# Kernel tuning notes

Measured on AMD Instinct MI355X. Metric: run time of the kernel, lower is better.

Reference implementation:

```python
import jax, jax.numpy as jnp
import numpy as np

N_HEAD = 12
N_EMBD = 768


def setup_inputs() -> dict:
    key = jax.random.key(0)
    k1, k2, k3, k4, k5 = jax.random.split(key, 5)
    B, T, C = 4, 2048, N_EMBD
    s = 0.02
    x = jax.random.normal(k1, (B, T, C), dtype=jnp.float32)
    w_attn = jax.random.normal(k2, (C, 3 * C), dtype=jnp.float32) * s
    b_attn = jnp.zeros((3 * C,), dtype=jnp.float32)
    w_proj = jax.random.normal(k3, (C, C), dtype=jnp.float32) * s
    b_proj = jnp.zeros((C,), dtype=jnp.float32)
    return {"x": x, "w_attn": w_attn, "b_attn": b_attn, "w_proj": w_proj, "b_proj": b_proj}


def reference(x, w_attn, b_attn, w_proj, b_proj):
    # dropout omitted (eval mode / dropout=0.0)
    B, T, C = x.shape
    H = N_HEAD
    D = C // H  # head dim
    qkv = x @ w_attn + b_attn                      # [B,T,3C]
    q, k, v = jnp.split(qkv, 3, axis=-1)
    q = q.reshape(B, T, H, D).transpose(0, 2, 1, 3)  # [B,H,T,D]
    k = k.reshape(B, T, H, D).transpose(0, 2, 1, 3)
    v = v.reshape(B, T, H, D).transpose(0, 2, 1, 3)
    att = jnp.einsum('bhqd,bhkd->bhqk', q, k) * (1.0 / np.sqrt(D))  # [B,H,T,T]
    causal = jnp.tril(jnp.ones((T, T), dtype=bool))
    att = jnp.where(causal[None, None], att, -jnp.inf)
    att = jax.nn.softmax(att, axis=-1)
    y = jnp.einsum('bhqk,bhkd->bhqd', att, v)      # [B,H,T,D]
    y = y.transpose(0, 2, 1, 3).reshape(B, T, C)
    return y @ w_proj + b_proj
```

## Files before the change

kernel.cpp:

```cpp
#include <hip/hip_runtime.h>
#include <stdint.h>

typedef unsigned short ushort_t;

#define T_SEQ 2048
#define BATCH 4
#define NHEAD 12
#define CEMB 768
#define HDIM 64
#define C3 2304

__device__ __forceinline__ ushort_t f2b_hw(float f) {
  union { __bf16 h; ushort_t u; } p;
  p.h = (__bf16)f;
  return p.u;
}
__device__ __forceinline__ uint32_t pkbf16(float lo, float hi) {
  union { __bf16 h[2]; uint32_t u; } p;
  p.h[0] = (__bf16)lo; p.h[1] = (__bf16)hi;
  return p.u;
}

typedef __attribute__((address_space(3))) unsigned int lds_u32_t;
typedef const __attribute__((address_space(1))) unsigned int glb_u32_t;
__device__ __forceinline__ void async_cp16(const void* g, void* l) {
  __builtin_amdgcn_global_load_lds((glb_u32_t*)g, (lds_u32_t*)l, 16, 0, 0);
}

__global__ __launch_bounds__(256) void prep_k(const float* __restrict__ x, ushort_t* __restrict__ xb,
                                              const float* __restrict__ wa, ushort_t* __restrict__ wT,
                                              const float* __restrict__ wp, ushort_t* __restrict__ wpT) {
  const int blk = blockIdx.x;
  const int tid = threadIdx.x;
  if (blk < 3072) {
    const int i = blk * 256 + tid;
    float4 a = ((const float4*)x)[2 * i];
    float4 b = ((const float4*)x)[2 * i + 1];
    uint4 v;
    v.x = pkbf16(a.x, a.y); v.y = pkbf16(a.z, a.w);
    v.z = pkbf16(b.x, b.y); v.w = pkbf16(b.z, b.w);
    ((uint4*)xb)[i] = v;
    return;
  }
  __shared__ ushort_t tile[32][33];
  const float* in; ushort_t* out; int R, C, bx, by;
  if (blk < 4800) {
    const int t = blk - 3072;
    in = wa; out = wT; R = CEMB; C = C3;
    bx = t % 72; by = t / 72;
  } else {
    const int t = blk - 4800;
    in = wp; out = wpT; R = CEMB; C = CEMB;
    bx = t % 24; by = t / 24;
  }
  const int tx = tid & 31, ty = tid >> 5;
  const int c0 = bx * 32, r0 = by * 32;
  for (int i = ty; i < 32; i += 8)
    tile[i][tx] = f2b_hw(in[(size_t)(r0 + i) * C + c0 + tx]);
  __syncthreads();
  for (int i = ty; i < 32; i += 8)
    out[(size_t)(c0 + i) * R + r0 + tx] = tile[tx][i];
}

typedef __bf16 bf16x8 __attribute__((ext_vector_type(8)));
typedef float f32x4 __attribute__((ext_vector_type(4)));

template <bool OUTF, int BM>
__global__ __launch_bounds__(256) void gemm_bt(const ushort_t* __restrict__ A,
                                               const ushort_t* __restrict__ Bt,
                                               const float* __restrict__ bias,
                                               void* __restrict__ Cv,
                                               int M, int N, int K) {
  constexpr int TM = BM / 32;
  __shared__ ushort_t As[2 * BM * 32];
  __shared__ ushort_t Bs[2 * 128 * 32];
  const int tid = threadIdx.x;
  const int m0 = blockIdx.y * BM, n0 = blockIdx.x * 128;
  const int wid = tid >> 6, lane = tid & 63;
  const int quad = lane >> 4, l15 = lane & 15;
  const int wm = (wid >> 1) * (BM / 2), wn = (wid & 1) * 64;
  f32x4 acc[TM][4] = {};

  const int e0 = tid * 8;
  const int r0s = e0 >> 5, c0s = e0 & 31;
  const int e1 = e0 + 2048;
  const int r1s = e1 >> 5, c1s = e1 & 31;

  for (int k0 = 0; k0 < K; k0 += 64) {
    __syncthreads();
#pragma unroll
    for (int p = 0; p < 2; p++) {
      const int kc = k0 + p * 32;
      async_cp16(&A[(size_t)(m0 + r0s) * K + kc + c0s], &As[p * BM * 32 + e0]);
      if constexpr (BM == 128)
        async_cp16(&A[(size_t)(m0 + r1s) * K + kc + c1s], &As[p * BM * 32 + e1]);
      async_cp16(&Bt[(size_t)(n0 + r0s) * K + kc + c0s], &Bs[p * 128 * 32 + e0]);
      async_cp16(&Bt[(size_t)(n0 + r1s) * K + kc + c1s], &Bs[p * 128 * 32 + e1]);
    }
    __syncthreads();
    bf16x8 af[TM][2], bfr[4][2];
#pragma unroll
    for (int t = 0; t < TM; t++)
#pragma unroll
      for (int p = 0; p < 2; p++)
        af[t][p] = *(const bf16x8*)&As[p * BM * 32 + (wm + t * 16 + l15) * 32 + quad * 8];
#pragma unroll
    for (int t = 0; t < 4; t++)
#pragma unroll
      for (int p = 0; p < 2; p++)
        bfr[t][p] = *(const bf16x8*)&Bs[p * 128 * 32 + (wn + t * 16 + l15) * 32 + quad * 8];
#pragma unroll
    for (int p = 0; p < 2; p++)
#pragma unroll
      for (int tm = 0; tm < TM; tm++)
#pragma unroll
        for (int tn = 0; tn < 4; tn++)
          acc[tm][tn] = __builtin_amdgcn_mfma_f32_16x16x32_bf16(af[tm][p], bfr[tn][p], acc[tm][tn], 0, 0, 0);
  }

#pragma unroll
  for (int tm = 0; tm < TM; tm++) {
    const int row = m0 + wm + tm * 16 + quad * 4;
#pragma unroll
    for (int tn = 0; tn < 4; tn++) {
      const int col = n0 + wn + tn * 16 + l15;
      const float bv = bias[col];
#pragma unroll
      for (int rr = 0; rr < 4; rr++) {
        if constexpr (OUTF)
          ((float*)Cv)[(size_t)(row + rr) * N + col] = acc[tm][tn][rr] + bv;
        else
          ((ushort_t*)Cv)[(size_t)(row + rr) * N + col] = f2b_hw(acc[tm][tn][rr] + bv);
      }
    }
  }
}

#define VSTR 64

__device__ __forceinline__ void commit_v(ushort_t* __restrict__ vt, const int* __restrict__ offs,
                                         uint4 pV0, uint4 pV1) {
  union { uint32_t u[4]; uint4 v; } a, c;
  a.v = pV0; c.v = pV1;
#pragma unroll
  for (int j = 0; j < 8; j++) {
    uint32_t pk = __builtin_amdgcn_perm(c.u[j >> 1], a.u[j >> 1],
                                        (j & 1) ? 0x07060302u : 0x05040100u);
    *(uint32_t*)&vt[offs[j]] = pk;
  }
}

__global__ __launch_bounds__(256) void attn_mfma_k(const ushort_t* __restrict__ qkv,
                                                   ushort_t* __restrict__ y) {
  __shared__ ushort_t Ksm[2][2][64 * 32];
  __shared__ ushort_t Vt[2][64 * VSTR];
  __shared__ ushort_t Plds[4][16 * VSTR];

  const int qt = 31 - blockIdx.y;
  const int h = blockIdx.x >> 2, b = blockIdx.x & 3;
  const int tid = threadIdx.x;
  const int w = tid >> 6, lane = tid & 63;
  const int quad = lane >> 4, l15 = lane & 15;
  const int nkt = qt + 1;
  const int qw = qt * 64 + w * 16;

  const int e0 = tid * 8;
  const int kchunk = (tid & 3) ^ ((tid >> 3) & 3);
  const ushort_t* kbase = qkv + ((size_t)(b * T_SEQ) + (tid >> 2)) * C3 + CEMB + h * HDIM + kchunk * 8;
  const int vpair = tid & 31, vd0 = (tid >> 5) * 8;
  const ushort_t* vbase = qkv + ((size_t)(b * T_SEQ) + 2 * vpair) * C3 + 2 * CEMB + h * HDIM + vd0;
  const size_t step = (size_t)64 * C3;

  int voffw[8];
#pragma unroll
  for (int j = 0; j < 8; j++)
    voffw[j] = (vd0 + j) * VSTR + (((vpair >> 2) ^ j) << 3) + ((vpair & 3) << 1);

  const int sw7 = l15 & 7;
  int koff[4];
#pragma unroll
  for (int m = 0; m < 4; m++)
    koff[m] = (m * 16 + l15) * 32 + ((quad ^ ((l15 >> 1) & 3)) << 3);
  int apoff[2];
#pragma unroll
  for (int kb = 0; kb < 2; kb++)
    apoff[kb] = l15 * VSTR + (((quad + 4 * kb) ^ sw7) << 3);
  int poffWm[4];
#pragma unroll
  for (int m = 0; m < 4; m++)
    poffWm[m] = l15 * VSTR + (((2 * m + (quad >> 1)) ^ sw7) << 3) + ((quad & 1) << 2);
  const int qloc = 16 * w + l15;

  const float C2 = 0.18033688011112042f;

  bf16x8 qB[2];
#pragma unroll
  for (int kb = 0; kb < 2; kb++)
    qB[kb] = *(const bf16x8*)&qkv[((size_t)(b * T_SEQ + qw + l15)) * C3 +
                                  h * HDIM + kb * 32 + quad * 8];

  f32x4 o2[4] = {};
  float m_i = -3e38f, l_i = 0.f;

  const ushort_t* kp = kbase;
  const ushort_t* vp = vbase;
  uint4 pV0 = *(const uint4*)vp, pV1 = *(const uint4*)(vp + C3);
  async_cp16(kp, &Ksm[0][0][e0]);
  async_cp16(kp + 32, &Ksm[0][1][e0]);
  commit_v(Vt[0], voffw, pV0, pV1);
  vp += step;
  pV0 = *(const uint4*)vp; pV1 = *(const uint4*)(vp + C3);

  for (int kt = 0; kt < nkt; ++kt) {
    __syncthreads();
    if (kt + 1 < nkt) {
      const int nb = (kt + 1) & 1;
      kp += step;
      async_cp16(kp, &Ksm[nb][0][e0]);
      async_cp16(kp + 32, &Ksm[nb][1][e0]);
      commit_v(Vt[nb], voffw, pV0, pV1);
      if (kt + 2 < nkt) {
        vp += step;
        pV0 = *(const uint4*)vp; pV1 = *(const uint4*)(vp + C3);
      }
    }
    const int cb = kt & 1;

    bf16x8 kA[4][2];
#pragma unroll
    for (int m = 0; m < 4; m++) {
      kA[m][0] = *(const bf16x8*)&Ksm[cb][0][koff[m]];
      kA[m][1] = *(const bf16x8*)&Ksm[cb][1][koff[m]];
    }
    f32x4 st[4] = {};
#pragma unroll
    for (int m = 0; m < 4; m++) {
      st[m] = __builtin_amdgcn_mfma_f32_16x16x32_bf16(kA[m][0], qB[0], st[m], 0, 0, 0);
      st[m] = __builtin_amdgcn_mfma_f32_16x16x32_bf16(kA[m][1], qB[1], st[m], 0, 0, 0);
    }

    if (kt == qt) {
#pragma unroll
      for (int m = 0; m < 4; m++)
#pragma unroll
        for (int r = 0; r < 4; r++)
          if (m * 16 + quad * 4 + r > qloc) st[m][r] = -3e38f;
    }

    f32x4 mq;
#pragma unroll
    for (int r = 0; r < 4; r++)
      mq[r] = fmaxf(fmaxf(st[0][r], st[1][r]), fmaxf(st[2][r], st[3][r]));
    const float mxl = fmaxf(fmaxf(mq[0], mq[1]), fmaxf(mq[2], mq[3]));

    float al = 1.f;
    if (!__all(mxl - m_i <= 22.18f)) {
      float mx = fmaxf(mxl, __shfl_xor(mxl, 16, 64));
      mx = fmaxf(mx, __shfl_xor(mx, 32, 64));
      const float mnew = fmaxf(m_i, mx);
      al = exp2f((m_i - mnew) * C2);
      m_i = mnew;
#pragma unroll
      for (int nd = 0; nd < 4; nd++)
#pragma unroll
        for (int r = 0; r < 4; r++) o2[nd][r] *= al;
    }
    const float mnc = m_i * C2;
#pragma unroll
    for (int m = 0; m < 4; m++)
#pragma unroll
      for (int r = 0; r < 4; r++)
        st[m][r] = exp2f(fmaf(st[m][r], C2, -mnc));
    f32x4 s4;
#pragma unroll
    for (int r = 0; r < 4; r++)
      s4[r] = (st[0][r] + st[1][r]) + (st[2][r] + st[3][r]);
    float ls = (s4[0] + s4[1]) + (s4[2] + s4[3]);
    ls += __shfl_xor(ls, 16, 64);
    ls += __shfl_xor(ls, 32, 64);
    l_i = l_i * al + ls;

#pragma unroll
    for (int m = 0; m < 4; m++) {
      uint2 pk;
      pk.x = pkbf16(st[m][0], st[m][1]);
      pk.y = pkbf16(st[m][2], st[m][3]);
      *(uint2*)&Plds[w][poffWm[m]] = pk;
    }

    asm volatile("s_waitcnt lgkmcnt(0)" ::: "memory");

    bf16x8 ap[2], bv[4][2];
#pragma unroll
    for (int kb = 0; kb < 2; kb++)
      ap[kb] = *(const bf16x8*)&Plds[w][apoff[kb]];
#pragma unroll
    for (int nd = 0; nd < 4; nd++)
#pragma unroll
      for (int kb = 0; kb < 2; kb++)
        bv[nd][kb] = *(const bf16x8*)&Vt[cb][nd * 1024 + apoff[kb]];
#pragma unroll
    for (int nd = 0; nd < 4; nd++) {
      o2[nd] = __builtin_amdgcn_mfma_f32_16x16x32_bf16(bv[nd][0], ap[0], o2[nd], 0, 0, 0);
      o2[nd] = __builtin_amdgcn_mfma_f32_16x16x32_bf16(bv[nd][1], ap[1], o2[nd], 0, 0, 0);
    }
  }

  {
    const float inv = 1.0f / l_i;
    const int qg = qw + l15;
    ushort_t* yp = y + ((size_t)(b * T_SEQ + qg)) * CEMB + h * HDIM + quad * 4;
#pragma unroll
    for (int nd = 0; nd < 4; nd++) {
      uint2 pk;
      pk.x = pkbf16(o2[nd][0] * inv, o2[nd][1] * inv);
      pk.y = pkbf16(o2[nd][2] * inv, o2[nd][3] * inv);
      *(uint2*)(yp + nd * 16) = pk;
    }
  }
}

extern "C" void kernel_launch(void* const* d_in, const int* in_sizes, int n_in,
                              void* d_out, int out_size, void* d_ws, size_t ws_size,
                              hipStream_t stream) {
  const float* x      = (const float*)d_in[0];
  const float* w_attn = (const float*)d_in[1];
  const float* b_attn = (const float*)d_in[2];
  const float* w_proj = (const float*)d_in[3];
  const float* b_proj = (const float*)d_in[4];
  float* out = (float*)d_out;

  char* ws = (char*)d_ws;
  ushort_t* qkv = (ushort_t*)ws;
  ushort_t* y   = qkv + (size_t)8192 * 2304;
  ushort_t* xb  = y + (size_t)8192 * 768;
  ushort_t* wT  = xb + (size_t)8192 * 768;
  ushort_t* wpT = wT + (size_t)2304 * 768;

  prep_k<<<5376, 256, 0, stream>>>(x, xb, w_attn, wT, w_proj, wpT);

  gemm_bt<false, 128><<<dim3(C3 / 128, 8192 / 128), 256, 0, stream>>>(xb, wT, b_attn, qkv, 8192, C3, CEMB);

  attn_mfma_k<<<dim3(48, 32), 256, 0, stream>>>(qkv, y);

  gemm_bt<true, 64><<<dim3(CEMB / 128, 8192 / 64), 256, 0, stream>>>(y, wpT, b_proj, out, 8192, CEMB, CEMB);
}
```

Before: 231.1 us.

## Process 128 queries per attention block, two 16-row fragments per wave

The attention kernel now gives each wave 32 query rows, as two 16-row fragments, so each block covers 128 queries. Each K/V tile staged in LDS is reused for twice as many queries, which halves the grid and the K/V global traffic per query. The row-sum reduction across lanes is deferred to the epilogue, and a launch-bounds occupancy hint is added. In exchange there is higher register and LDS pressure, fewer blocks for load balancing across the causal triangle, and wasted masked work on the last two diagonal tiles.

```diff
diff --git a/kernel.cpp b/kernel.cpp
--- a/kernel.cpp
+++ b/kernel.cpp
@@ -150,19 +150,19 @@
   }
 }
 
-__global__ __launch_bounds__(256) void attn_mfma_k(const ushort_t* __restrict__ qkv,
-                                                   ushort_t* __restrict__ y) {
+__global__ __launch_bounds__(256, 3) void attn_mfma_k(const ushort_t* __restrict__ qkv,
+                                                      ushort_t* __restrict__ y) {
   __shared__ ushort_t Ksm[2][2][64 * 32];
   __shared__ ushort_t Vt[2][64 * VSTR];
-  __shared__ ushort_t Plds[4][16 * VSTR];
-
-  const int qt = 31 - blockIdx.y;
+  __shared__ ushort_t Plds[4][32 * VSTR];
+
+  const int qt = 15 - blockIdx.y;
   const int h = blockIdx.x >> 2, b = blockIdx.x & 3;
   const int tid = threadIdx.x;
   const int w = tid >> 6, lane = tid & 63;
   const int quad = lane >> 4, l15 = lane & 15;
-  const int nkt = qt + 1;
-  const int qw = qt * 64 + w * 16;
+  const int nkt = 2 * qt + 2;
+  const int qw = qt * 128 + w * 32;
 
   const int e0 = tid * 8;
   const int kchunk = (tid & 3) ^ ((tid >> 3) & 3);
@@ -181,26 +181,33 @@
 #pragma unroll
   for (int m = 0; m < 4; m++)
     koff[m] = (m * 16 + l15) * 32 + ((quad ^ ((l15 >> 1) & 3)) << 3);
-  int apoff[2];
+  int vroff[2];
 #pragma unroll
   for (int kb = 0; kb < 2; kb++)
-    apoff[kb] = l15 * VSTR + (((quad + 4 * kb) ^ sw7) << 3);
-  int poffWm[4];
-#pragma unroll
-  for (int m = 0; m < 4; m++)
-    poffWm[m] = l15 * VSTR + (((2 * m + (quad >> 1)) ^ sw7) << 3) + ((quad & 1) << 2);
-  const int qloc = 16 * w + l15;
+    vroff[kb] = l15 * VSTR + (((quad + 4 * kb) ^ sw7) << 3);
+  int poffW[2][4];
+#pragma unroll
+  for (int qf = 0; qf < 2; qf++)
+#pragma unroll
+    for (int m = 0; m < 4; m++)
+      poffW[qf][m] = (qf * 16 + l15) * VSTR + (((2 * m + (quad >> 1)) ^ sw7) << 3) + ((quad & 1) << 2);
+
+  const int qrel0 = w * 32 + l15;
+  const int qrel1 = qrel0 + 16;
 
   const float C2 = 0.18033688011112042f;
 
-  bf16x8 qB[2];
-#pragma unroll
-  for (int kb = 0; kb < 2; kb++)
-    qB[kb] = *(const bf16x8*)&qkv[((size_t)(b * T_SEQ + qw + l15)) * C3 +
-                                  h * HDIM + kb * 32 + quad * 8];
-
-  f32x4 o2[4] = {};
-  float m_i = -3e38f, l_i = 0.f;
+  bf16x8 qB[2][2];
+#pragma unroll
+  for (int qf = 0; qf < 2; qf++)
+#pragma unroll
+    for (int kb = 0; kb < 2; kb++)
+      qB[qf][kb] = *(const bf16x8*)&qkv[((size_t)(b * T_SEQ + qw + qf * 16 + l15)) * C3 +
+                                        h * HDIM + kb * 32 + quad * 8];
+
+  f32x4 o2[2][4] = {};
+  float m0 = -3e38f, m1 = -3e38f;
+  float lq0 = 0.f, lq1 = 0.f;
 
   const ushort_t* kp = kbase;
   const ushort_t* vp = vbase;
@@ -232,90 +239,123 @@
       kA[m][0] = *(const bf16x8*)&Ksm[cb][0][koff[m]];
       kA[m][1] = *(const bf16x8*)&Ksm[cb][1][koff[m]];
     }
-    f32x4 st[4] = {};
+    f32x4 st0[4] = {}, st1[4] = {};
 #pragma unroll
     for (int m = 0; m < 4; m++) {
-      st[m] = __builtin_amdgcn_mfma_f32_16x16x32_bf16(kA[m][0], qB[0], st[m], 0, 0, 0);
-      st[m] = __builtin_amdgcn_mfma_f32_16x16x32_bf16(kA[m][1], qB[1], st[m], 0, 0, 0);
-    }
-
-    if (kt == qt) {
+      st0[m] = __builtin_amdgcn_mfma_f32_16x16x32_bf16(kA[m][0], qB[0][0], st0[m], 0, 0, 0);
+      st0[m] = __builtin_amdgcn_mfma_f32_16x16x32_bf16(kA[m][1], qB[0][1], st0[m], 0, 0, 0);
+      st1[m] = __builtin_amdgcn_mfma_f32_16x16x32_bf16(kA[m][0], qB[1][0], st1[m], 0, 0, 0);
+      st1[m] = __builtin_amdgcn_mfma_f32_16x16x32_bf16(kA[m][1], qB[1][1], st1[m], 0, 0, 0);
+    }
+
+    if (kt >= nkt - 2) {
+      const int krel = (kt << 6) - (qt << 7) + quad * 4;
 #pragma unroll
       for (int m = 0; m < 4; m++)
 #pragma unroll
-        for (int r = 0; r < 4; r++)
-          if (m * 16 + quad * 4 + r > qloc) st[m][r] = -3e38f;
-    }
-
-    f32x4 mq;
-#pragma unroll
-    for (int r = 0; r < 4; r++)
-      mq[r] = fmaxf(fmaxf(st[0][r], st[1][r]), fmaxf(st[2][r], st[3][r]));
-    const float mxl = fmaxf(fmaxf(mq[0], mq[1]), fmaxf(mq[2], mq[3]));
-
-    float al = 1.f;
-    if (!__all(mxl - m_i <= 22.18f)) {
-      float mx = fmaxf(mxl, __shfl_xor(mxl, 16, 64));
-      mx = fmaxf(mx, __shfl_xor(mx, 32, 64));
-      const float mnew = fmaxf(m_i, mx);
-      al = exp2f((m_i - mnew) * C2);
-      m_i = mnew;
+        for (int r = 0; r < 4; r++) {
+          const int kr = krel + m * 16 + r;
+          if (kr > qrel0) st0[m][r] = -3e38f;
+          if (kr > qrel1) st1[m][r] = -3e38f;
+        }
+    }
+
+    f32x4 mq0, mq1;
+#pragma unroll
+    for (int r = 0; r < 4; r++) {
+      mq0[r] = fmaxf(fmaxf(st0[0][r], st0[1][r]), fmaxf(st0[2][r], st0[3][r]));
+      mq1[r] = fmaxf(fmaxf(st1[0][r], st1[1][r]), fmaxf(st1[2][r], st1[3][r]));
+    }
+    const float mx0 = fmaxf(fmaxf(mq0[0], mq0[1]), fmaxf(mq0[2], mq0[3]));
+    const float mx1 = fmaxf(fmaxf(mq1[0], mq1[1]), fmaxf(mq1[2], mq1[3]));
+
+    float al0 = 1.f, al1 = 1.f;
+    const bool viol = (mx0 - m0 > 22.18f) || (mx1 - m1 > 22.18f);
+    if (__any(viol)) {
+      float a = fmaxf(mx0, __shfl_xor(mx0, 16, 64));
+      a = fmaxf(a, __shfl_xor(a, 32, 64));
+      float bm = fmaxf(mx1, __shfl_xor(mx1, 16, 64));
+      bm = fmaxf(bm, __shfl_xor(bm, 32, 64));
+      const float n0 = fmaxf(m0, a), n1 = fmaxf(m1, bm);
+      al0 = exp2f((m0 - n0) * C2);
+      al1 = exp2f((m1 - n1) * C2);
+      m0 = n0; m1 = n1;
 #pragma unroll
       for (int nd = 0; nd < 4; nd++)
 #pragma unroll
-        for (int r = 0; r < 4; r++) o2[nd][r] *= al;
-    }
-    const float mnc = m_i * C2;
+        for (int r = 0; r < 4; r++) {
+          o2[0][nd][r] *= al0;
+          o2[1][nd][r] *= al1;
+        }
+    }
+    const float mnc0 = m0 * C2, mnc1 = m1 * C2;
 #pragma unroll
     for (int m = 0; m < 4; m++)
 #pragma unroll
-      for (int r = 0; r < 4; r++)
-        st[m][r] = exp2f(fmaf(st[m][r], C2, -mnc));
-    f32x4 s4;
-#pragma unroll
-    for (int r = 0; r < 4; r++)
-      s4[r] = (st[0][r] + st[1][r]) + (st[2][r] + st[3][r]);
-    float ls = (s4[0] + s4[1]) + (s4[2] + s4[3]);
-    ls += __shfl_xor(ls, 16, 64);
-    ls += __shfl_xor(ls, 32, 64);
-    l_i = l_i * al + ls;
+      for (int r = 0; r < 4; r++) {
+        st0[m][r] = exp2f(fmaf(st0[m][r], C2, -mnc0));
+        st1[m][r] = exp2f(fmaf(st1[m][r], C2, -mnc1));
+      }
+    f32x4 s40, s41;
+#pragma unroll
+    for (int r = 0; r < 4; r++) {
+      s40[r] = (st0[0][r] + st0[1][r]) + (st0[2][r] + st0[3][r]);
+      s41[r] = (st1[0][r] + st1[1][r]) + (st1[2][r] + st1[3][r]);
+    }
+    lq0 = fmaf(lq0, al0, (s40[0] + s40[1]) + (s40[2] + s40[3]));
+    lq1 = fmaf(lq1, al1, (s41[0] + s41[1]) + (s41[2] + s41[3]));
 
 #pragma unroll
     for (int m = 0; m < 4; m++) {
-      uint2 pk;
-      pk.x = pkbf16(st[m][0], st[m][1]);
-      pk.y = pkbf16(st[m][2], st[m][3]);
-      *(uint2*)&Plds[w][poffWm[m]] = pk;
+      uint2 pk0, pk1;
+      pk0.x = pkbf16(st0[m][0], st0[m][1]);
+      pk0.y = pkbf16(st0[m][2], st0[m][3]);
+      pk1.x = pkbf16(st1[m][0], st1[m][1]);
+      pk1.y = pkbf16(st1[m][2], st1[m][3]);
+      *(uint2*)&Plds[w][poffW[0][m]] = pk0;
+      *(uint2*)&Plds[w][poffW[1][m]] = pk1;
     }
 
     asm volatile("s_waitcnt lgkmcnt(0)" ::: "memory");
 
-    bf16x8 ap[2], bv[4][2];
-#pragma unroll
-    for (int kb = 0; kb < 2; kb++)
-      ap[kb] = *(const bf16x8*)&Plds[w][apoff[kb]];
+    bf16x8 ap0[2], ap1[2], bvf[4][2];
+#pragma unroll
+    for (int kb = 0; kb < 2; kb++) {
+      ap0[kb] = *(const bf16x8*)&Plds[w][vroff[kb]];
+      ap1[kb] = *(const bf16x8*)&Plds[w][vroff[kb] + 16 * VSTR];
+    }
 #pragma unroll
     for (int nd = 0; nd < 4; nd++)
 #pragma unroll
       for (int kb = 0; kb < 2; kb++)
-        bv[nd][kb] = *(const bf16x8*)&Vt[cb][nd * 1024 + apoff[kb]];
+        bvf[nd][kb] = *(const bf16x8*)&Vt[cb][nd * 1024 + vroff[kb]];
 #pragma unroll
     for (int nd = 0; nd < 4; nd++) {
-      o2[nd] = __builtin_amdgcn_mfma_f32_16x16x32_bf16(bv[nd][0], ap[0], o2[nd], 0, 0, 0);
-      o2[nd] = __builtin_amdgcn_mfma_f32_16x16x32_bf16(bv[nd][1], ap[1], o2[nd], 0, 0, 0);
+      o2[0][nd] = __builtin_amdgcn_mfma_f32_16x16x32_bf16(bvf[nd][0], ap0[0], o2[0][nd], 0, 0, 0);
+      o2[0][nd] = __builtin_amdgcn_mfma_f32_16x16x32_bf16(bvf[nd][1], ap0[1], o2[0][nd], 0, 0, 0);
+      o2[1][nd] = __builtin_amdgcn_mfma_f32_16x16x32_bf16(bvf[nd][0], ap1[0], o2[1][nd], 0, 0, 0);
+      o2[1][nd] = __builtin_amdgcn_mfma_f32_16x16x32_bf16(bvf[nd][1], ap1[1], o2[1][nd], 0, 0, 0);
     }
   }
 
   {
-    const float inv = 1.0f / l_i;
-    const int qg = qw + l15;
-    ushort_t* yp = y + ((size_t)(b * T_SEQ + qg)) * CEMB + h * HDIM + quad * 4;
-#pragma unroll
-    for (int nd = 0; nd < 4; nd++) {
-      uint2 pk;
-      pk.x = pkbf16(o2[nd][0] * inv, o2[nd][1] * inv);
-      pk.y = pkbf16(o2[nd][2] * inv, o2[nd][3] * inv);
-      *(uint2*)(yp + nd * 16) = pk;
+    float lt0 = lq0 + __shfl_xor(lq0, 16, 64);
+    lt0 += __shfl_xor(lt0, 32, 64);
+    float lt1 = lq1 + __shfl_xor(lq1, 16, 64);
+    lt1 += __shfl_xor(lt1, 32, 64);
+    const float inv0 = 1.0f / lt0, inv1 = 1.0f / lt1;
+#pragma unroll
+    for (int qf = 0; qf < 2; qf++) {
+      const float inv = qf ? inv1 : inv0;
+      const int qg = qw + qf * 16 + l15;
+      ushort_t* yp = y + ((size_t)(b * T_SEQ + qg)) * CEMB + h * HDIM + quad * 4;
+#pragma unroll
+      for (int nd = 0; nd < 4; nd++) {
+        uint2 pk;
+        pk.x = pkbf16(o2[qf][nd][0] * inv, o2[qf][nd][1] * inv);
+        pk.y = pkbf16(o2[qf][nd][2] * inv, o2[qf][nd][3] * inv);
+        *(uint2*)(yp + nd * 16) = pk;
+      }
     }
   }
 }
@@ -341,7 +381,7 @@
 
   gemm_bt<false, 128><<<dim3(C3 / 128, 8192 / 128), 256, 0, stream>>>(xb, wT, b_attn, qkv, 8192, C3, CEMB);
 
-  attn_mfma_k<<<dim3(48, 32), 256, 0, stream>>>(qkv, y);
+  attn_mfma_k<<<dim3(48, 16), 256, 0, stream>>>(qkv, y);
 
   gemm_bt<true, 64><<<dim3(CEMB / 128, 8192 / 64), 256, 0, stream>>>(y, wpT, b_proj, out, 8192, CEMB, CEMB);
 }
```

Measured after the change: 215.9 us. -6.6%, faster.
